# Kernel tuning notes

Measured on AMD Instinct MI355X. Metric: run time of the kernel, lower is better.

Reference implementation:

```python
import jax, jax.numpy as jnp
import numpy as np

WS = 8        # window size (square)
TW = 8        # total windows per side = input_resolution // WS
NH = 16       # num heads


def make_indices(ws, tw):
    # local relative position index (N, N)
    c = np.stack(np.meshgrid(np.arange(ws), np.arange(ws), indexing='ij')).reshape(2, -1)
    rel = (c[:, :, None] - c[:, None, :]).transpose(1, 2, 0).astype(np.int64)
    rel[..., 0] += ws - 1
    rel[..., 1] += ws - 1
    rel[..., 0] *= 2 * ws - 1
    local_idx = rel.sum(-1)
    # global (window-token -> window-grid) relative position index (N, tw*tw)
    ck = np.stack(np.meshgrid(np.arange(tw), np.arange(tw), indexing='ij')).reshape(2, -1)
    relg = (c[:, :, None] - ck[:, None, :]).transpose(1, 2, 0).astype(np.int64)
    relg[..., 0] += tw - 1
    relg[..., 1] += tw - 1
    relg[..., 0] *= ws + tw - 1
    global_idx = relg.sum(-1)
    return local_idx, global_idx


def setup_inputs() -> dict:
    key = jax.random.key(0)
    ks = jax.random.split(key, 13)
    B, H, W, C = 16, 64, 64, 512
    s = 0.02
    return {
        'x': jax.random.normal(ks[0], (B, H, W, C), jnp.float32),
        'qkv_w': jax.random.normal(ks[1], (C, 3 * C), jnp.float32) * s,
        'qkv_b': jax.random.normal(ks[2], (3 * C,), jnp.float32) * s,
        'local_bias_table': jax.random.normal(ks[3], ((2 * WS - 1) ** 2, NH), jnp.float32) * s,
        'global_bias_table': jax.random.normal(ks[4], ((WS + TW - 1) ** 2, NH), jnp.float32) * s,
        'local_proj_w': jax.random.normal(ks[5], (C, C), jnp.float32) * s,
        'local_proj_b': jax.random.normal(ks[6], (C,), jnp.float32) * s,
        'pool_w': jnp.full((WS * WS,), 1.0 / (WS * WS) * (WS * WS), jnp.float32) * 0 + jax.random.normal(ks[7], (WS * WS,), jnp.float32) * s + 1.0 / (WS * WS),
        'pool_b': jnp.zeros((1,), jnp.float32),
        'global_proj_w': jax.random.normal(ks[8], (C, C), jnp.float32) * s,
        'global_proj_b': jax.random.normal(ks[9], (C,), jnp.float32) * s,
        'pfc_w': jax.random.normal(ks[10], (2 * C, C), jnp.float32) * s,
        'pfc_b': jax.random.normal(ks[11], (C,), jnp.float32) * s,
    }


def reference(x, qkv_w, qkv_b, local_bias_table, global_bias_table,
              local_proj_w, local_proj_b, pool_w, pool_b,
              global_proj_w, global_proj_b, pfc_w, pfc_b):
    B, H, W, C = x.shape
    N = WS * WS                      # tokens per window
    nWs = (H // WS) * (W // WS)      # number of windows
    B_ = B * nWs
    hd = C // NH
    scale = hd ** -0.5

    local_idx, global_idx = make_indices(WS, H // WS)

    # NOTE: faithful to original — qkv applied to x in row-major order,
    # then reshaped into (B_, N, ...) chunks (window_partition output is unused).
    qkv = (x.reshape(-1, C) @ qkv_w + qkv_b).reshape(B_, N, 3, NH, hd)
    qkv = qkv.transpose(2, 0, 3, 1, 4)  # (3, B_, NH, N, hd)
    q, k, v = qkv[0], qkv[1], qkv[2]

    # ---- fine (local window) attention ----
    lb = local_bias_table[local_idx.reshape(-1)].reshape(N, N, NH).transpose(2, 0, 1)
    fine = jax.nn.softmax(jnp.einsum('bhnd,bhmd->bhnm', q * scale, k) + lb[None])
    fine_out = jnp.einsum('bhnm,bhmd->bnhd', fine, v).reshape(B_, N, C)
    fine_out = fine_out @ local_proj_w + local_proj_b

    # ---- coarse (pooled global) attention ----
    k5 = k.reshape(B, nWs, NH, N, hd)
    v5 = v.reshape(B, nWs, NH, N, hd)
    # pooled over the N window-token axis; original uses pool_layer_k for BOTH K and V
    Kg = jnp.einsum('bwhnd,n->bhwd', k5, pool_w) + pool_b  # (B, NH, nWs, hd)
    Vg = jnp.einsum('bwhnd,n->bhwd', v5, pool_w) + pool_b
    Kb = jnp.broadcast_to(Kg[:, None], (B, nWs, NH, nWs, hd)).reshape(B_, NH, nWs, hd)
    Vb = jnp.broadcast_to(Vg[:, None], (B, nWs, NH, nWs, hd)).reshape(B_, NH, nWs, hd)

    gb = global_bias_table[global_idx.reshape(-1)].reshape(N, nWs, NH).transpose(2, 0, 1)
    coarse = jax.nn.softmax(jnp.einsum('bhnd,bhwd->bhnw', q * scale, Kb) + gb[None])
    coarse_out = jnp.einsum('bhnw,bhwd->bnhd', coarse, Vb).reshape(B_, N, C)
    coarse_out = coarse_out @ global_proj_w + global_proj_b

    # ---- fused projection ----
    out = jnp.concatenate([fine_out, coarse_out], axis=-1) @ pfc_w + pfc_b
    return out  # (B_, N, C)
```

## Files before the change

### kernel.cpp

```cpp
#include <hip/hip_runtime.h>


typedef unsigned int u32;
typedef _Float16 f16;
typedef __attribute__((ext_vector_type(8))) _Float16 f16x8;
typedef __attribute__((ext_vector_type(4))) float f32x4;

__device__ __forceinline__ f32x4 mfma_16x16x32(f16x8 a, f16x8 b, f32x4 c) {
  return __builtin_amdgcn_mfma_f32_16x16x32_f16(a, b, c, 0, 0, 0);
}

__device__ __forceinline__ void async_cp16(const void* g, void* l) {
  __builtin_amdgcn_global_load_lds(
      (const __attribute__((address_space(1))) u32*)g,
      (__attribute__((address_space(3))) u32*)l, 16, 0, 0);
}


__global__ void k_cvtx(const float* __restrict__ X, f16* __restrict__ X16) {
  const size_t stride = (size_t)2048 * 256 * 8;
  size_t base = ((size_t)blockIdx.x * 256 + threadIdx.x) * 8;
  for (int it = 0; it < 8; ++it, base += stride) {
    const float4 a = *reinterpret_cast<const float4*>(X + base);
    const float4 b = *reinterpret_cast<const float4*>(X + base + 4);
    f16x8 r;
    r[0] = (f16)a.x; r[1] = (f16)a.y; r[2] = (f16)a.z; r[3] = (f16)a.w;
    r[4] = (f16)b.x; r[5] = (f16)b.y; r[6] = (f16)b.z; r[7] = (f16)b.w;
    *reinterpret_cast<f16x8*>(X16 + base) = r;
  }
}

__global__ void k_biastab(const float* __restrict__ ltab, const float* __restrict__ gtab,
                          float* __restrict__ lbf, float* __restrict__ gbf) {
  const int id = blockIdx.x * 256 + threadIdx.x;
  const int pair = id & 4095;
  const int n = pair >> 6, m = pair & 63;
  const int yn = n >> 3, xn = n & 7;
  const int ym = m >> 3, xm = m & 7;
  const int idx = (yn - ym + 7) * 15 + (xn - xm + 7);
  if (id < 4096) {
#pragma unroll
    for (int h = 0; h < 16; ++h) lbf[h * 4096 + pair] = ltab[idx * 16 + h];
  } else {
#pragma unroll
    for (int h = 0; h < 16; ++h) gbf[h * 4096 + pair] = gtab[idx * 16 + h];
  }
}

__global__ void k_tqkvw(const float* __restrict__ w, f16* __restrict__ wT) {
  __shared__ f16 sT[64][72];
  const int bid = blockIdx.x;
  const int k0 = (bid / 24) * 64, n0 = (bid % 24) * 64;
  const int t = threadIdx.x;
#pragma unroll
  for (int p = 0; p < 4; ++p) {
    const int kl = p * 16 + (t >> 4), nl = (t & 15) * 4;
    const float4 v = *reinterpret_cast<const float4*>(w + (size_t)(k0 + kl) * 1536 + n0 + nl);
    sT[kl][nl] = (f16)v.x; sT[kl][nl + 1] = (f16)v.y;
    sT[kl][nl + 2] = (f16)v.z; sT[kl][nl + 3] = (f16)v.w;
  }
  __syncthreads();
#pragma unroll
  for (int q = 0; q < 2; ++q) {
    const int nl = q * 32 + (t >> 3), kl = (t & 7) * 8;
    f16x8 r;
#pragma unroll
    for (int j = 0; j < 8; ++j) r[j] = sT[kl + j][nl];
    *reinterpret_cast<f16x8*>(wT + (size_t)(n0 + nl) * 512 + k0 + kl) = r;
  }
}

__global__ __launch_bounds__(256) void k_compose(const float* __restrict__ lpw,
                                                 const float* __restrict__ gpw,
                                                 const float* __restrict__ pfc_w,
                                                 f16* __restrict__ WT) {
  __shared__ float sW[16][16];
  const int kk0 = blockIdx.x * 16;
  const bool top = kk0 < 512;
  const float* src = top ? (lpw + kk0 * 512) : (gpw + (kk0 - 512) * 512);
  const float* pf = pfc_w + (top ? 0 : 512 * 512);
  const int t = threadIdx.x;
  float acc0[16], acc1[16];
#pragma unroll
  for (int i = 0; i < 16; ++i) { acc0[i] = 0.f; acc1[i] = 0.f; }
  for (int ct = 0; ct < 32; ++ct) {
    sW[t >> 4][t & 15] = src[(t >> 4) * 512 + ct * 16 + (t & 15)];
    __syncthreads();
#pragma unroll
    for (int cc = 0; cc < 16; ++cc) {
      const int c = ct * 16 + cc;
      const float p0 = pf[c * 512 + t];
      const float p1 = pf[c * 512 + t + 256];
#pragma unroll
      for (int i = 0; i < 16; ++i) { acc0[i] += sW[i][cc] * p0; acc1[i] += sW[i][cc] * p1; }
    }
    __syncthreads();
  }
#pragma unroll
  for (int i = 0; i < 16; ++i) WT[(size_t)t * 1024 + kk0 + i] = (f16)acc0[i];
#pragma unroll
  for (int i = 0; i < 16; ++i) WT[(size_t)(t + 256) * 1024 + kk0 + i] = (f16)acc1[i];
}

__global__ void k_bc_init(const float* __restrict__ pfc_b, float* __restrict__ bc) {
  const int j = blockIdx.x * 256 + threadIdx.x;
  bc[j] = pfc_b[j];
}

__global__ void k_bc_acc(const float* __restrict__ lpb, const float* __restrict__ gpb,
                         const float* __restrict__ pfc_w, float* __restrict__ bc) {
  const int t = threadIdx.x;
  const int c0 = blockIdx.x * 32;
  float p0 = 0.f, p1 = 0.f;
#pragma unroll
  for (int i = 0; i < 32; ++i) {
    const int c = c0 + i;
    const float wgt = (c < 512) ? lpb[c] : gpb[c - 512];
    p0 += wgt * pfc_w[(size_t)c * 512 + t];
    p1 += wgt * pfc_w[(size_t)c * 512 + t + 256];
  }
  atomicAdd(bc + t, p0);
  atomicAdd(bc + t + 256, p1);
}

__global__ __launch_bounds__(512) void k_gemm_qkv(const f16* __restrict__ A,
                                                  const f16* __restrict__ BT,
                                                  const float* __restrict__ qkv_b,
                                                  f16* __restrict__ qb,
                                                  f16* __restrict__ kb,
                                                  f16* __restrict__ vb) {
  __shared__ f16 sA[8192], sB[4096];
  const int wid = (blockIdx.x & 7) * 384 + (blockIdx.x >> 3);
  const int br = wid / 12, bn = wid % 12;
  const int t = threadIdx.x;
  const int wv = t >> 6, l = t & 63, lr = l & 15, lk = l >> 4;
  const int wvr = wv >> 1, wvc = wv & 1;

  f32x4 acc[4][4] = {};

  const f16* gA = A + (size_t)(br * 256 + (t >> 2)) * 512 + (t & 3) * 8;
  const f16* gB = BT + (size_t)(bn * 128 + (t >> 2)) * 512 + (t & 3) * 8;

  for (int kk = 0; kk < 16; ++kk) {
    async_cp16(gA + kk * 32, &sA[t * 8]);
    async_cp16(gA + 128 * 512 + kk * 32, &sA[4096 + t * 8]);
    async_cp16(gB + kk * 32, &sB[t * 8]);
    __syncthreads();
    f16x8 af[4], bf[4];
#pragma unroll
    for (int m = 0; m < 4; ++m)
      af[m] = *reinterpret_cast<const f16x8*>(&sA[(wvr * 64 + m * 16 + lr) * 32 + lk * 8]);
#pragma unroll
    for (int n = 0; n < 4; ++n)
      bf[n] = *reinterpret_cast<const f16x8*>(&sB[(wvc * 64 + n * 16 + lr) * 32 + lk * 8]);
#pragma unroll
    for (int m = 0; m < 4; ++m)
#pragma unroll
      for (int n = 0; n < 4; ++n) acc[m][n] = mfma_16x16x32(af[m], bf[n], acc[m][n]);
    __syncthreads();
  }

#pragma unroll
  for (int n = 0; n < 4; ++n) {
    const int col = bn * 128 + wvc * 64 + n * 16 + lr;
    const int which = col >> 9;
    const int hh = (col >> 5) & 15;
    const int d = col & 31;
    f16* dst = which == 0 ? qb : (which == 1 ? kb : vb);
    const float bias = qkv_b[col];
#pragma unroll
    for (int m = 0; m < 4; ++m)
#pragma unroll
      for (int r = 0; r < 4; ++r) {
        const int row = br * 256 + wvr * 64 + m * 16 + lk * 4 + r;
        dst[(size_t)(((row >> 6) << 4) + hh) * 2048 + (row & 63) * 32 + d] =
            (f16)(acc[m][n][r] + bias);
      }
  }
}

__global__ void k_pool(const f16* __restrict__ kb, const f16* __restrict__ vb,
                       const float* __restrict__ pool_w, const float* __restrict__ pool_b,
                       f16* __restrict__ Kgb, f16* __restrict__ Vgt) {
  const int bid = blockIdx.x;
  const int w = bid & 63, h = (bid >> 6) & 15, b = bid >> 10;
  const int d = threadIdx.x & 31;
  const f16* src = (threadIdx.x < 32 ? kb : vb) + (size_t)((b * 64 + w) * 16 + h) * 2048;
  float acc = 0.f;
#pragma unroll 8
  for (int n = 0; n < 64; ++n) acc += (float)src[n * 32 + d] * pool_w[n];
  acc += pool_b[0];
  if (threadIdx.x < 32)
    Kgb[(size_t)bid * 32 + d] = (f16)acc;
  else
    Vgt[((size_t)(b * 16 + h) * 32 + d) * 64 + w] = (f16)acc;
}

__device__ __forceinline__ void attn_half(const f16x8 aq, const f16* sKm, const f16* sVm,
                                          const float* __restrict__ btab, f16* sP,
                                          const int wv, const int lr, const int lk,
                                          f16* __restrict__ catp) {
  const float scale = 0.17677669529663687f;
  f32x4 s[4] = {};
#pragma unroll
  for (int j = 0; j < 4; ++j)
    s[j] = mfma_16x16x32(aq, *reinterpret_cast<const f16x8*>(&sKm[(j * 16 + lr) * 32 + lk * 8]), s[j]);

  const float* bt = btab + (wv * 16 + lk * 4) * 64;
  float p[4][4], inv[4];
#pragma unroll
  for (int r = 0; r < 4; ++r) {
    float m = -1e30f;
#pragma unroll
    for (int j = 0; j < 4; ++j) {
      const float v = s[j][r] * scale + bt[r * 64 + j * 16 + lr];
      p[j][r] = v;
      m = fmaxf(m, v);
    }
    m = fmaxf(m, __shfl_xor(m, 1));
    m = fmaxf(m, __shfl_xor(m, 2));
    m = fmaxf(m, __shfl_xor(m, 4));
    m = fmaxf(m, __shfl_xor(m, 8));
    float su = 0.f;
#pragma unroll
    for (int j = 0; j < 4; ++j) {
      const float e = __expf(p[j][r] - m);
      p[j][r] = e;
      su += e;
    }
    su += __shfl_xor(su, 1);
    su += __shfl_xor(su, 2);
    su += __shfl_xor(su, 4);
    su += __shfl_xor(su, 8);
    inv[r] = 1.f / su;
  }
#pragma unroll
  for (int r = 0; r < 4; ++r)
#pragma unroll
    for (int j = 0; j < 4; ++j)
      sP[(wv * 16 + lk * 4 + r) * 64 + j * 16 + lr] = (f16)p[j][r];

  const f16x8 a0 = *reinterpret_cast<const f16x8*>(&sP[(wv * 16 + lr) * 64 + lk * 8]);
  const f16x8 a1 = *reinterpret_cast<const f16x8*>(&sP[(wv * 16 + lr) * 64 + 32 + lk * 8]);
#pragma unroll
  for (int n = 0; n < 2; ++n) {
    f32x4 o = {};
    o = mfma_16x16x32(a0, *reinterpret_cast<const f16x8*>(&sVm[(n * 16 + lr) * 64 + lk * 8]), o);
    o = mfma_16x16x32(a1, *reinterpret_cast<const f16x8*>(&sVm[(n * 16 + lr) * 64 + 32 + lk * 8]), o);
#pragma unroll
    for (int r = 0; r < 4; ++r)
      catp[(size_t)(wv * 16 + lk * 4 + r) * 1024 + n * 16 + lr] = (f16)(o[r] * inv[r]);
  }
}

__global__ __launch_bounds__(256) void k_attn(const f16* __restrict__ qb,
                                              const f16* __restrict__ kb,
                                              const f16* __restrict__ vb,
                                              const f16* __restrict__ Kgb,
                                              const f16* __restrict__ Vgt,
                                              const float* __restrict__ lbf,
                                              const float* __restrict__ gbf,
                                              f16* __restrict__ cat) {
  __shared__ f16 sQ[2048], sK[2048], sVt[2048], sKg[2048], sVgt[2048], sP[4096];
  const int bid = blockIdx.x;
  const int b_ = bid >> 4, h = bid & 15;
  const int gslice = ((b_ >> 6) << 4) + h;
  const int t = threadIdx.x;
  const int wv = t >> 6, l = t & 63, lr = l & 15, lk = l >> 4;

  async_cp16(qb + (size_t)bid * 2048 + t * 8, &sQ[t * 8]);
  async_cp16(kb + (size_t)bid * 2048 + t * 8, &sK[t * 8]);
  async_cp16(vb + (size_t)bid * 2048 + t * 8, &sP[t * 8]);
  async_cp16(Kgb + (size_t)gslice * 2048 + t * 8, &sKg[t * 8]);
  async_cp16(Vgt + (size_t)gslice * 2048 + t * 8, &sVgt[t * 8]);
  __syncthreads();

  {
    const int d = t >> 3, n0 = (t & 7) << 3;
    f16x8 wr;
#pragma unroll
    for (int j = 0; j < 8; ++j) wr[j] = sP[(n0 + j) * 32 + d];
    *reinterpret_cast<f16x8*>(&sVt[d * 64 + n0]) = wr;
  }
  __syncthreads();

  const f16x8 aq = *reinterpret_cast<const f16x8*>(&sQ[(wv * 16 + lr) * 32 + lk * 8]);
  f16* catp = cat + (size_t)b_ * 64 * 1024 + h * 32;

  attn_half(aq, sK, sVt, lbf + h * 4096, sP, wv, lr, lk, catp);
  attn_half(aq, sKg, sVgt, gbf + h * 4096, sP, wv, lr, lk, catp + 512);
}

__global__ __launch_bounds__(512) void k_gemm_final(const f16* __restrict__ A,
                                                    const f16* __restrict__ BT,
                                                    const float* __restrict__ bc,
                                                    float* __restrict__ out) {
  __shared__ f16 sA[8192], sB[4096];
  const int wid = (blockIdx.x & 7) * 128 + (blockIdx.x >> 3);
  const int br = wid >> 2, bn = wid & 3;
  const int t = threadIdx.x;
  const int wv = t >> 6, l = t & 63, lr = l & 15, lk = l >> 4;
  const int wvr = wv >> 1, wvc = wv & 1;

  f32x4 acc[4][4] = {};

  const f16* gA = A + (size_t)(br * 256 + (t >> 2)) * 1024 + (t & 3) * 8;
  const f16* gB = BT + (size_t)(bn * 128 + (t >> 2)) * 1024 + (t & 3) * 8;

  for (int kk = 0; kk < 32; ++kk) {
    async_cp16(gA + kk * 32, &sA[t * 8]);
    async_cp16(gA + (size_t)128 * 1024 + kk * 32, &sA[4096 + t * 8]);
    async_cp16(gB + kk * 32, &sB[t * 8]);
    __syncthreads();
    f16x8 af[4], bf[4];
#pragma unroll
    for (int m = 0; m < 4; ++m)
      af[m] = *reinterpret_cast<const f16x8*>(&sA[(wvr * 64 + m * 16 + lr) * 32 + lk * 8]);
#pragma unroll
    for (int n = 0; n < 4; ++n)
      bf[n] = *reinterpret_cast<const f16x8*>(&sB[(wvc * 64 + n * 16 + lr) * 32 + lk * 8]);
#pragma unroll
    for (int m = 0; m < 4; ++m)
#pragma unroll
      for (int n = 0; n < 4; ++n) acc[m][n] = mfma_16x16x32(af[m], bf[n], acc[m][n]);
    __syncthreads();
  }

#pragma unroll
  for (int n = 0; n < 4; ++n) {
    const int col = bn * 128 + wvc * 64 + n * 16 + lr;
    const float bias = bc[col];
#pragma unroll
    for (int m = 0; m < 4; ++m)
#pragma unroll
      for (int r = 0; r < 4; ++r) {
        const int row = br * 256 + wvr * 64 + m * 16 + lk * 4 + r;
        out[(size_t)row * 512 + col] = acc[m][n][r] + bias;
      }
  }
}


extern "C" void kernel_launch(void* const* d_in, const int* in_sizes, int n_in,
                              void* d_out, int out_size, void* d_ws, size_t ws_size,
                              hipStream_t stream) {
  const float* x      = (const float*)d_in[0];
  const float* qkv_w  = (const float*)d_in[1];
  const float* qkv_b  = (const float*)d_in[2];
  const float* ltab   = (const float*)d_in[3];
  const float* gtab   = (const float*)d_in[4];
  const float* lpw    = (const float*)d_in[5];
  const float* lpb    = (const float*)d_in[6];
  const float* pool_w = (const float*)d_in[7];
  const float* pool_b = (const float*)d_in[8];
  const float* gpw    = (const float*)d_in[9];
  const float* gpb    = (const float*)d_in[10];
  const float* pfc_w  = (const float*)d_in[11];
  const float* pfc_b  = (const float*)d_in[12];
  float* out = (float*)d_out;

  char* ws = (char*)d_ws;
  f16*   qb   = (f16*)(ws + 0);
  f16*   kb   = (f16*)(ws + 67108864);
  f16*   vb   = (f16*)(ws + 134217728);
  f16*   cat  = (f16*)(ws + 201326592);
  f16*   X16  = (f16*)(ws + 201326592);
  f16*   qwT  = (f16*)(ws + 335544320);
  f16*   WcT  = (f16*)(ws + 337117184);
  float* bc   = (float*)(ws + 338165760);
  float* lbf  = (float*)(ws + 338167808);
  float* gbf  = (float*)(ws + 338429952);
  f16*   Kgb  = (f16*)(ws + 338692096);
  f16*   Vgt  = (f16*)(ws + 339740672);

  k_cvtx<<<2048, 256, 0, stream>>>(x, X16);
  k_biastab<<<32, 256, 0, stream>>>(ltab, gtab, lbf, gbf);
  k_tqkvw<<<192, 256, 0, stream>>>(qkv_w, qwT);
  k_compose<<<64, 256, 0, stream>>>(lpw, gpw, pfc_w, WcT);
  k_bc_init<<<2, 256, 0, stream>>>(pfc_b, bc);
  k_bc_acc<<<32, 256, 0, stream>>>(lpb, gpb, pfc_w, bc);
  k_gemm_qkv<<<3072, 512, 0, stream>>>(X16, qwT, qkv_b, qb, kb, vb);
  k_pool<<<16384, 64, 0, stream>>>(kb, vb, pool_w, pool_b, Kgb, Vgt);
  k_attn<<<16384, 256, 0, stream>>>(qb, kb, vb, Kgb, Vgt, lbf, gbf, cat);
  k_gemm_final<<<1024, 512, 0, stream>>>(cat, WcT, bc, out);
}
```

Measured before the change: 533.8 us.

## Fuse fp32 conversion and pooling into QKV GEMM; fuse attention with output projection

The QKV GEMM now loads fp32 x directly into LDS through a swizzled layout and converts to fp16 with round-toward-zero packing. This removes the separate conversion kernel and its extra 64MB round trip. K/V window pooling is computed in the GEMM epilogue with cross-lane reductions, which replaces the pooling kernel. Attention and the final composed projection are merged into one per-window kernel that loops over heads and accumulates the output GEMM from a shared-memory concat tile. This avoids writing and rereading the concat buffer, at the cost of lower parallelism (1024 blocks), 16 serialized head iterations with three barriers each, and doubled LDS use for A.

```diff
diff --git a/kernel.cpp b/kernel.cpp
--- a/kernel.cpp
+++ b/kernel.cpp
@@ -2,9 +2,12 @@
 
 
 typedef unsigned int u32;
+typedef unsigned short u16;
 typedef _Float16 f16;
 typedef __attribute__((ext_vector_type(8))) _Float16 f16x8;
 typedef __attribute__((ext_vector_type(4))) float f32x4;
+typedef __fp16 fp16x2 __attribute__((ext_vector_type(2)));
+typedef __attribute__((ext_vector_type(4))) u32 u32x4;
 
 __device__ __forceinline__ f32x4 mfma_16x16x32(f16x8 a, f16x8 b, f32x4 c) {
   return __builtin_amdgcn_mfma_f32_16x16x32_f16(a, b, c, 0, 0, 0);
@@ -16,19 +19,15 @@
       (__attribute__((address_space(3))) u32*)l, 16, 0, 0);
 }
 
-
-__global__ void k_cvtx(const float* __restrict__ X, f16* __restrict__ X16) {
-  const size_t stride = (size_t)2048 * 256 * 8;
-  size_t base = ((size_t)blockIdx.x * 256 + threadIdx.x) * 8;
-  for (int it = 0; it < 8; ++it, base += stride) {
-    const float4 a = *reinterpret_cast<const float4*>(X + base);
-    const float4 b = *reinterpret_cast<const float4*>(X + base + 4);
-    f16x8 r;
-    r[0] = (f16)a.x; r[1] = (f16)a.y; r[2] = (f16)a.z; r[3] = (f16)a.w;
-    r[4] = (f16)b.x; r[5] = (f16)b.y; r[6] = (f16)b.z; r[7] = (f16)b.w;
-    *reinterpret_cast<f16x8*>(X16 + base) = r;
-  }
-}
+__device__ __forceinline__ f16x8 cvt8_rtz(const float4 a, const float4 b) {
+  u32x4 w;
+  w[0] = __builtin_bit_cast(u32, __builtin_amdgcn_cvt_pkrtz(a.x, a.y));
+  w[1] = __builtin_bit_cast(u32, __builtin_amdgcn_cvt_pkrtz(a.z, a.w));
+  w[2] = __builtin_bit_cast(u32, __builtin_amdgcn_cvt_pkrtz(b.x, b.y));
+  w[3] = __builtin_bit_cast(u32, __builtin_amdgcn_cvt_pkrtz(b.z, b.w));
+  return __builtin_bit_cast(f16x8, w);
+}
+
 
 __global__ void k_biastab(const float* __restrict__ ltab, const float* __restrict__ gtab,
                           float* __restrict__ lbf, float* __restrict__ gbf) {
@@ -123,13 +122,18 @@
   atomicAdd(bc + t + 256, p1);
 }
 
-__global__ __launch_bounds__(512) void k_gemm_qkv(const f16* __restrict__ A,
-                                                  const f16* __restrict__ BT,
-                                                  const float* __restrict__ qkv_b,
-                                                  f16* __restrict__ qb,
-                                                  f16* __restrict__ kb,
-                                                  f16* __restrict__ vb) {
-  __shared__ f16 sA[8192], sB[4096];
+__global__ __launch_bounds__(512, 2) void k_gemm_qkv(const float* __restrict__ X,
+                                                     const f16* __restrict__ BT,
+                                                     const float* __restrict__ qkv_b,
+                                                     const float* __restrict__ pool_w,
+                                                     const float* __restrict__ pool_b,
+                                                     f16* __restrict__ qb,
+                                                     f16* __restrict__ kb,
+                                                     f16* __restrict__ vb,
+                                                     f16* __restrict__ Kgb,
+                                                     f16* __restrict__ Vgt) {
+  __shared__ float sA[8192];
+  __shared__ f16 sB[4096];
   const int wid = (blockIdx.x & 7) * 384 + (blockIdx.x >> 3);
   const int br = wid / 12, bn = wid % 12;
   const int t = threadIdx.x;
@@ -138,36 +142,56 @@
 
   f32x4 acc[4][4] = {};
 
-  const f16* gA = A + (size_t)(br * 256 + (t >> 2)) * 512 + (t & 3) * 8;
-  const f16* gB = BT + (size_t)(bn * 128 + (t >> 2)) * 512 + (t & 3) * 8;
+  const int arow = t >> 3;
+  const int afc = ((t & 7) ^ (arow & 7)) * 4;
+  const float* gA = X + (size_t)(br * 256 + arow) * 512 + afc;
+  const int brow = t >> 2;
+  const int bfc = ((t & 3) ^ (brow & 3)) * 8;
+  const f16* gB = BT + (size_t)(bn * 128 + brow) * 512 + bfc;
 
   for (int kk = 0; kk < 16; ++kk) {
-    async_cp16(gA + kk * 32, &sA[t * 8]);
-    async_cp16(gA + 128 * 512 + kk * 32, &sA[4096 + t * 8]);
+#pragma unroll
+    for (int i = 0; i < 4; ++i)
+      async_cp16(gA + (size_t)(i * 64) * 512 + kk * 32, &sA[(i * 512 + t) * 4]);
     async_cp16(gB + kk * 32, &sB[t * 8]);
     __syncthreads();
     f16x8 af[4], bf[4];
 #pragma unroll
+    for (int m = 0; m < 4; ++m) {
+      const int row = wvr * 64 + m * 16 + lr;
+      const int c0 = (2 * lk) ^ (lr & 7), c1 = (2 * lk + 1) ^ (lr & 7);
+      const float4 v0 = *reinterpret_cast<const float4*>(&sA[row * 32 + c0 * 4]);
+      const float4 v1 = *reinterpret_cast<const float4*>(&sA[row * 32 + c1 * 4]);
+      af[m] = cvt8_rtz(v0, v1);
+    }
+#pragma unroll
+    for (int n = 0; n < 4; ++n) {
+      const int row = wvc * 64 + n * 16 + lr;
+      bf[n] = *reinterpret_cast<const f16x8*>(&sB[row * 32 + ((lk ^ (lr & 3)) * 8)]);
+    }
+#pragma unroll
     for (int m = 0; m < 4; ++m)
-      af[m] = *reinterpret_cast<const f16x8*>(&sA[(wvr * 64 + m * 16 + lr) * 32 + lk * 8]);
-#pragma unroll
-    for (int n = 0; n < 4; ++n)
-      bf[n] = *reinterpret_cast<const f16x8*>(&sB[(wvc * 64 + n * 16 + lr) * 32 + lk * 8]);
-#pragma unroll
-    for (int m = 0; m < 4; ++m)
 #pragma unroll
       for (int n = 0; n < 4; ++n) acc[m][n] = mfma_16x16x32(af[m], bf[n], acc[m][n]);
     __syncthreads();
   }
+
+  const int w_idx = br * 4 + wvr;
+  const int bb = w_idx >> 6, ww = w_idx & 63;
+  float pw[4][4];
+#pragma unroll
+  for (int m = 0; m < 4; ++m)
+#pragma unroll
+    for (int r = 0; r < 4; ++r) pw[m][r] = pool_w[m * 16 + lk * 4 + r];
+  const float pb = pool_b[0];
 
 #pragma unroll
   for (int n = 0; n < 4; ++n) {
     const int col = bn * 128 + wvc * 64 + n * 16 + lr;
     const int which = col >> 9;
-    const int hh = (col >> 5) & 15;
-    const int d = col & 31;
+    const int hh = (col >> 5) & 15, d = col & 31;
+    const float bias = qkv_b[col];
     f16* dst = which == 0 ? qb : (which == 1 ? kb : vb);
-    const float bias = qkv_b[col];
 #pragma unroll
     for (int m = 0; m < 4; ++m)
 #pragma unroll
@@ -176,165 +200,177 @@
         dst[(size_t)(((row >> 6) << 4) + hh) * 2048 + (row & 63) * 32 + d] =
             (f16)(acc[m][n][r] + bias);
       }
-  }
-}
-
-__global__ void k_pool(const f16* __restrict__ kb, const f16* __restrict__ vb,
-                       const float* __restrict__ pool_w, const float* __restrict__ pool_b,
-                       f16* __restrict__ Kgb, f16* __restrict__ Vgt) {
-  const int bid = blockIdx.x;
-  const int w = bid & 63, h = (bid >> 6) & 15, b = bid >> 10;
-  const int d = threadIdx.x & 31;
-  const f16* src = (threadIdx.x < 32 ? kb : vb) + (size_t)((b * 64 + w) * 16 + h) * 2048;
-  float acc = 0.f;
-#pragma unroll 8
-  for (int n = 0; n < 64; ++n) acc += (float)src[n * 32 + d] * pool_w[n];
-  acc += pool_b[0];
-  if (threadIdx.x < 32)
-    Kgb[(size_t)bid * 32 + d] = (f16)acc;
-  else
-    Vgt[((size_t)(b * 16 + h) * 32 + d) * 64 + w] = (f16)acc;
-}
-
-__device__ __forceinline__ void attn_half(const f16x8 aq, const f16* sKm, const f16* sVm,
-                                          const float* __restrict__ btab, f16* sP,
-                                          const int wv, const int lr, const int lk,
-                                          f16* __restrict__ catp) {
-  const float scale = 0.17677669529663687f;
-  f32x4 s[4] = {};
-#pragma unroll
-  for (int j = 0; j < 4; ++j)
-    s[j] = mfma_16x16x32(aq, *reinterpret_cast<const f16x8*>(&sKm[(j * 16 + lr) * 32 + lk * 8]), s[j]);
-
-  const float* bt = btab + (wv * 16 + lk * 4) * 64;
-  float p[4][4], inv[4];
-#pragma unroll
-  for (int r = 0; r < 4; ++r) {
-    float m = -1e30f;
-#pragma unroll
-    for (int j = 0; j < 4; ++j) {
-      const float v = s[j][r] * scale + bt[r * 64 + j * 16 + lr];
-      p[j][r] = v;
-      m = fmaxf(m, v);
-    }
-    m = fmaxf(m, __shfl_xor(m, 1));
-    m = fmaxf(m, __shfl_xor(m, 2));
-    m = fmaxf(m, __shfl_xor(m, 4));
-    m = fmaxf(m, __shfl_xor(m, 8));
-    float su = 0.f;
-#pragma unroll
-    for (int j = 0; j < 4; ++j) {
-      const float e = __expf(p[j][r] - m);
-      p[j][r] = e;
-      su += e;
-    }
-    su += __shfl_xor(su, 1);
-    su += __shfl_xor(su, 2);
-    su += __shfl_xor(su, 4);
-    su += __shfl_xor(su, 8);
-    inv[r] = 1.f / su;
-  }
-#pragma unroll
-  for (int r = 0; r < 4; ++r)
-#pragma unroll
-    for (int j = 0; j < 4; ++j)
-      sP[(wv * 16 + lk * 4 + r) * 64 + j * 16 + lr] = (f16)p[j][r];
-
-  const f16x8 a0 = *reinterpret_cast<const f16x8*>(&sP[(wv * 16 + lr) * 64 + lk * 8]);
-  const f16x8 a1 = *reinterpret_cast<const f16x8*>(&sP[(wv * 16 + lr) * 64 + 32 + lk * 8]);
-#pragma unroll
-  for (int n = 0; n < 2; ++n) {
-    f32x4 o = {};
-    o = mfma_16x16x32(a0, *reinterpret_cast<const f16x8*>(&sVm[(n * 16 + lr) * 64 + lk * 8]), o);
-    o = mfma_16x16x32(a1, *reinterpret_cast<const f16x8*>(&sVm[(n * 16 + lr) * 64 + 32 + lk * 8]), o);
-#pragma unroll
-    for (int r = 0; r < 4; ++r)
-      catp[(size_t)(wv * 16 + lk * 4 + r) * 1024 + n * 16 + lr] = (f16)(o[r] * inv[r]);
-  }
-}
-
-__global__ __launch_bounds__(256) void k_attn(const f16* __restrict__ qb,
-                                              const f16* __restrict__ kb,
-                                              const f16* __restrict__ vb,
-                                              const f16* __restrict__ Kgb,
-                                              const f16* __restrict__ Vgt,
-                                              const float* __restrict__ lbf,
-                                              const float* __restrict__ gbf,
-                                              f16* __restrict__ cat) {
-  __shared__ f16 sQ[2048], sK[2048], sVt[2048], sKg[2048], sVgt[2048], sP[4096];
-  const int bid = blockIdx.x;
-  const int b_ = bid >> 4, h = bid & 15;
-  const int gslice = ((b_ >> 6) << 4) + h;
+    if (which != 0) {
+      float part = 0.f;
+#pragma unroll
+      for (int m = 0; m < 4; ++m)
+#pragma unroll
+        for (int r = 0; r < 4; ++r) part += (acc[m][n][r] + bias) * pw[m][r];
+      part += __shfl_xor(part, 16);
+      part += __shfl_xor(part, 32);
+      part += pb;
+      if (lk == 0) {
+        if (which == 1)
+          Kgb[((size_t)(bb * 16 + hh) * 64 + ww) * 32 + d] = (f16)part;
+        else
+          Vgt[((size_t)(bb * 16 + hh) * 32 + d) * 64 + ww] = (f16)part;
+      }
+    }
+  }
+}
+
+__global__ __launch_bounds__(512, 2) void k_attn_proj(const f16* __restrict__ qb,
+                                                      const f16* __restrict__ kb,
+                                                      const f16* __restrict__ vb,
+                                                      const f16* __restrict__ Kgb,
+                                                      const f16* __restrict__ Vgt,
+                                                      const float* __restrict__ lbf,
+                                                      const float* __restrict__ gbf,
+                                                      const f16* __restrict__ WcT,
+                                                      const float* __restrict__ bc,
+                                                      float* __restrict__ out) {
+  __shared__ f16 sVraw[2048];
+  __shared__ f16 sVt[2048];
+  __shared__ f16 sP[8192];
+  __shared__ f16 sCat[4096];
+  const int b_ = blockIdx.x;
+  const int b = b_ >> 6;
   const int t = threadIdx.x;
   const int wv = t >> 6, l = t & 63, lr = l & 15, lk = l >> 4;
-
-  async_cp16(qb + (size_t)bid * 2048 + t * 8, &sQ[t * 8]);
-  async_cp16(kb + (size_t)bid * 2048 + t * 8, &sK[t * 8]);
-  async_cp16(vb + (size_t)bid * 2048 + t * 8, &sP[t * 8]);
-  async_cp16(Kgb + (size_t)gslice * 2048 + t * 8, &sKg[t * 8]);
-  async_cp16(Vgt + (size_t)gslice * 2048 + t * 8, &sVgt[t * 8]);
-  __syncthreads();
-
-  {
-    const int d = t >> 3, n0 = (t & 7) << 3;
-    f16x8 wr;
-#pragma unroll
-    for (int j = 0; j < 8; ++j) wr[j] = sP[(n0 + j) * 32 + d];
-    *reinterpret_cast<f16x8*>(&sVt[d * 64 + n0]) = wr;
-  }
-  __syncthreads();
-
-  const f16x8 aq = *reinterpret_cast<const f16x8*>(&sQ[(wv * 16 + lr) * 32 + lk * 8]);
-  f16* catp = cat + (size_t)b_ * 64 * 1024 + h * 32;
-
-  attn_half(aq, sK, sVt, lbf + h * 4096, sP, wv, lr, lk, catp);
-  attn_half(aq, sKg, sVgt, gbf + h * 4096, sP, wv, lr, lk, catp + 512);
-}
-
-__global__ __launch_bounds__(512) void k_gemm_final(const f16* __restrict__ A,
-                                                    const f16* __restrict__ BT,
-                                                    const float* __restrict__ bc,
-                                                    float* __restrict__ out) {
-  __shared__ f16 sA[8192], sB[4096];
-  const int wid = (blockIdx.x & 7) * 128 + (blockIdx.x >> 3);
-  const int br = wid >> 2, bn = wid & 3;
-  const int t = threadIdx.x;
-  const int wv = t >> 6, l = t & 63, lr = l & 15, lk = l >> 4;
-  const int wvr = wv >> 1, wvc = wv & 1;
-
-  f32x4 acc[4][4] = {};
-
-  const f16* gA = A + (size_t)(br * 256 + (t >> 2)) * 1024 + (t & 3) * 8;
-  const f16* gB = BT + (size_t)(bn * 128 + (t >> 2)) * 1024 + (t & 3) * 8;
-
-  for (int kk = 0; kk < 32; ++kk) {
-    async_cp16(gA + kk * 32, &sA[t * 8]);
-    async_cp16(gA + (size_t)128 * 1024 + kk * 32, &sA[4096 + t * 8]);
-    async_cp16(gB + kk * 32, &sB[t * 8]);
-    __syncthreads();
-    f16x8 af[4], bf[4];
-#pragma unroll
-    for (int m = 0; m < 4; ++m)
-      af[m] = *reinterpret_cast<const f16x8*>(&sA[(wvr * 64 + m * 16 + lr) * 32 + lk * 8]);
-#pragma unroll
-    for (int n = 0; n < 4; ++n)
-      bf[n] = *reinterpret_cast<const f16x8*>(&sB[(wvc * 64 + n * 16 + lr) * 32 + lk * 8]);
-#pragma unroll
-    for (int m = 0; m < 4; ++m)
-#pragma unroll
-      for (int n = 0; n < 4; ++n) acc[m][n] = mfma_16x16x32(af[m], bf[n], acc[m][n]);
-    __syncthreads();
-  }
-
-#pragma unroll
-  for (int n = 0; n < 4; ++n) {
-    const int col = bn * 128 + wvc * 64 + n * 16 + lr;
+  const int wvq = wv & 3;
+  const bool fine = wv < 4;
+  const int wvM = wv & 1, wvN = wv >> 1;
+  const float scale = 0.17677669529663687f;
+
+  f32x4 acc[2][8] = {};
+
+  for (int h = 0; h < 16; ++h) {
+    const size_t hs = ((size_t)b_ * 16 + h) * 2048;
+    const size_t gs = ((size_t)b * 16 + h);
+    if (t < 256) async_cp16(vb + hs + t * 8, &sVraw[t * 8]);
+    __syncthreads();
+    if (t < 256) {
+      const int d = t >> 3, tok0 = (t & 7) << 3;
+      f16x8 w;
+#pragma unroll
+      for (int j = 0; j < 8; ++j) w[j] = sVraw[(tok0 + j) * 32 + d];
+      *reinterpret_cast<f16x8*>(&sVt[d * 64 + (((t & 7) ^ (d & 7)) << 3)]) = w;
+    }
+
+    const f16x8 aq = *reinterpret_cast<const f16x8*>(qb + hs + (wvq * 16 + lr) * 32 + lk * 8);
+    float p[4][4], inv[4];
+    {
+      f32x4 s[4];
+#pragma unroll
+      for (int j = 0; j < 4; ++j) {
+        const f16x8 bk = fine
+            ? *reinterpret_cast<const f16x8*>(kb + hs + (j * 16 + lr) * 32 + lk * 8)
+            : *reinterpret_cast<const f16x8*>(Kgb + (gs * 64 + j * 16 + lr) * 32 + lk * 8);
+        f32x4 z = {};
+        s[j] = mfma_16x16x32(aq, bk, z);
+      }
+      const float* bt = (fine ? lbf : gbf) + h * 4096 + (wvq * 16 + lk * 4) * 64;
+#pragma unroll
+      for (int r = 0; r < 4; ++r) {
+        float m = -1e30f;
+#pragma unroll
+        for (int j = 0; j < 4; ++j) {
+          const float v = s[j][r] * scale + bt[r * 64 + j * 16 + lr];
+          p[j][r] = v;
+          m = fmaxf(m, v);
+        }
+        m = fmaxf(m, __shfl_xor(m, 1));
+        m = fmaxf(m, __shfl_xor(m, 2));
+        m = fmaxf(m, __shfl_xor(m, 4));
+        m = fmaxf(m, __shfl_xor(m, 8));
+        float su = 0.f;
+#pragma unroll
+        for (int j = 0; j < 4; ++j) {
+          const float e = __expf(p[j][r] - m);
+          p[j][r] = e;
+          su += e;
+        }
+        su += __shfl_xor(su, 1);
+        su += __shfl_xor(su, 2);
+        su += __shfl_xor(su, 4);
+        su += __shfl_xor(su, 8);
+        inv[r] = 1.f / su;
+      }
+    }
+#pragma unroll
+    for (int r = 0; r < 4; ++r) {
+      const int rowP = wv * 16 + lk * 4 + r;
+#pragma unroll
+      for (int j = 0; j < 4; ++j) {
+        const int col = j * 16 + lr;
+        sP[rowP * 64 + (((col >> 3) ^ (rowP & 7)) << 3) + (col & 7)] = (f16)p[j][r];
+      }
+    }
+    __syncthreads();
+
+    {
+      const int rowP = wv * 16 + lr;
+      const f16x8 a0 = *reinterpret_cast<const f16x8*>(&sP[rowP * 64 + ((lk ^ (lr & 7)) << 3)]);
+      const f16x8 a1 = *reinterpret_cast<const f16x8*>(&sP[rowP * 64 + (((4 + lk) ^ (lr & 7)) << 3)]);
+#pragma unroll
+      for (int n = 0; n < 2; ++n) {
+        f16x8 b0, b1;
+        if (fine) {
+          const int d = n * 16 + lr;
+          b0 = *reinterpret_cast<const f16x8*>(&sVt[d * 64 + ((lk ^ (d & 7)) << 3)]);
+          b1 = *reinterpret_cast<const f16x8*>(&sVt[d * 64 + (((4 + lk) ^ (d & 7)) << 3)]);
+        } else {
+          const f16* vp = Vgt + (gs * 32 + n * 16 + lr) * 64 + lk * 8;
+          b0 = *reinterpret_cast<const f16x8*>(vp);
+          b1 = *reinterpret_cast<const f16x8*>(vp + 32);
+        }
+        f32x4 o = {};
+        o = mfma_16x16x32(a0, b0, o);
+        o = mfma_16x16x32(a1, b1, o);
+#pragma unroll
+        for (int r = 0; r < 4; ++r) {
+          const int rowC = wvq * 16 + lk * 4 + r;
+          const int colC = (fine ? 0 : 32) + n * 16 + lr;
+          sCat[rowC * 64 + (((colC >> 3) ^ (rowC & 7)) << 3) + (colC & 7)] =
+              (f16)(o[r] * inv[r]);
+        }
+      }
+    }
+    __syncthreads();
+
+    f16x8 a[2][2];
+#pragma unroll
+    for (int m = 0; m < 2; ++m) {
+      const int rowA = wvM * 32 + m * 16 + lr;
+#pragma unroll
+      for (int kh = 0; kh < 2; ++kh)
+        a[m][kh] = *reinterpret_cast<const f16x8*>(
+            &sCat[rowA * 64 + (((kh * 4 + lk) ^ (rowA & 7)) << 3)]);
+    }
+#pragma unroll
+    for (int n = 0; n < 8; ++n) {
+      const int col = wvN * 128 + n * 16 + lr;
+      const f16* wp = WcT + (size_t)col * 1024 + h * 32 + lk * 8;
+      const f16x8 b0 = *reinterpret_cast<const f16x8*>(wp);
+      const f16x8 b1 = *reinterpret_cast<const f16x8*>(wp + 512);
+#pragma unroll
+      for (int m = 0; m < 2; ++m) {
+        acc[m][n] = mfma_16x16x32(a[m][0], b0, acc[m][n]);
+        acc[m][n] = mfma_16x16x32(a[m][1], b1, acc[m][n]);
+      }
+    }
+    __syncthreads();
+  }
+
+#pragma unroll
+  for (int n = 0; n < 8; ++n) {
+    const int col = wvN * 128 + n * 16 + lr;
     const float bias = bc[col];
 #pragma unroll
-    for (int m = 0; m < 4; ++m)
+    for (int m = 0; m < 2; ++m)
 #pragma unroll
       for (int r = 0; r < 4; ++r) {
-        const int row = br * 256 + wvr * 64 + m * 16 + lk * 4 + r;
+        const int row = b_ * 64 + wvM * 32 + m * 16 + lk * 4 + r;
         out[(size_t)row * 512 + col] = acc[m][n][r] + bias;
       }
   }
@@ -363,24 +399,20 @@
   f16*   qb   = (f16*)(ws + 0);
   f16*   kb   = (f16*)(ws + 67108864);
   f16*   vb   = (f16*)(ws + 134217728);
-  f16*   cat  = (f16*)(ws + 201326592);
-  f16*   X16  = (f16*)(ws + 201326592);
-  f16*   qwT  = (f16*)(ws + 335544320);
-  f16*   WcT  = (f16*)(ws + 337117184);
-  float* bc   = (float*)(ws + 338165760);
-  float* lbf  = (float*)(ws + 338167808);
-  float* gbf  = (float*)(ws + 338429952);
-  f16*   Kgb  = (f16*)(ws + 338692096);
-  f16*   Vgt  = (f16*)(ws + 339740672);
-
-  k_cvtx<<<2048, 256, 0, stream>>>(x, X16);
+  f16*   qwT  = (f16*)(ws + 201326592);
+  f16*   WcT  = (f16*)(ws + 202899456);
+  float* bc   = (float*)(ws + 203948032);
+  float* lbf  = (float*)(ws + 203950080);
+  float* gbf  = (float*)(ws + 204212224);
+  f16*   Kgb  = (f16*)(ws + 204474368);
+  f16*   Vgt  = (f16*)(ws + 205522944);
+
   k_biastab<<<32, 256, 0, stream>>>(ltab, gtab, lbf, gbf);
   k_tqkvw<<<192, 256, 0, stream>>>(qkv_w, qwT);
   k_compose<<<64, 256, 0, stream>>>(lpw, gpw, pfc_w, WcT);
   k_bc_init<<<2, 256, 0, stream>>>(pfc_b, bc);
   k_bc_acc<<<32, 256, 0, stream>>>(lpb, gpb, pfc_w, bc);
-  k_gemm_qkv<<<3072, 512, 0, stream>>>(X16, qwT, qkv_b, qb, kb, vb);
-  k_pool<<<16384, 64, 0, stream>>>(kb, vb, pool_w, pool_b, Kgb, Vgt);
-  k_attn<<<16384, 256, 0, stream>>>(qb, kb, vb, Kgb, Vgt, lbf, gbf, cat);
-  k_gemm_final<<<1024, 512, 0, stream>>>(cat, WcT, bc, out);
-}
+  k_gemm_qkv<<<3072, 512, 0, stream>>>(x, qwT, qkv_b, pool_w, pool_b,
+                                       qb, kb, vb, Kgb, Vgt);
+  k_attn_proj<<<1024, 512, 0, stream>>>(qb, kb, vb, Kgb, Vgt, lbf, gbf, WcT, bc, out);
+}
```

Measured after the change: 898.3 us. 68.3% more time.
